# Performance work log

Measured on AMD Instinct MI355X. Metric: run time of the kernel, lower is better.

The kernel has to match this reference:

```python
import jax, jax.numpy as jnp
import numpy as np
import math

EMBED_DIM = 512
DEPTH = 0
HEAD_DIM = EMBED_DIM // 2
LAMBDA_INIT = 0.8 - 0.6 * math.exp(-0.3 * DEPTH)
RMS_EPS = 1e-5


def setup_inputs() -> dict:
    key = jax.random.key(0)
    ks = jax.random.split(key, 10)
    B, NG, NS, E = 8, 4096, 1024, EMBED_DIM
    s = 1.0 / math.sqrt(E)
    return {
        "gene": jax.random.normal(ks[0], (B, NG, E), jnp.float32),
        "substructure": jax.random.normal(ks[1], (B, NS, E), jnp.float32),
        "Wq": jax.random.normal(ks[2], (E, E), jnp.float32) * s,
        "Wk": jax.random.normal(ks[3], (E, E), jnp.float32) * s,
        "Wv": jax.random.normal(ks[4], (E, E), jnp.float32) * s,
        "Wo": jax.random.normal(ks[5], (E, E), jnp.float32) * s,
        "lambda_q1": jax.random.normal(ks[6], (HEAD_DIM,), jnp.float32) * 0.1,
        "lambda_k1": jax.random.normal(ks[7], (HEAD_DIM,), jnp.float32) * 0.1,
        "lambda_q2": jax.random.normal(ks[8], (HEAD_DIM,), jnp.float32) * 0.1,
        "lambda_k2": jax.random.normal(ks[9], (HEAD_DIM,), jnp.float32) * 0.1,
        "rms_weight": jnp.ones((E,), jnp.float32),
    }


def reference(gene, substructure, Wq, Wk, Wv, Wo,
              lambda_q1, lambda_k1, lambda_q2, lambda_k2, rms_weight):
    B, NG, E = gene.shape
    NS = substructure.shape[1]
    h = HEAD_DIM
    scaling = h ** -0.5

    # projections (torch Linear: y = x @ W.T)
    q = (gene @ Wq.T).reshape(B, NG, 2, h).transpose(0, 2, 1, 3)          # [B,2,NG,h]
    k = (substructure @ Wk.T).reshape(B, NS, 2, h).transpose(0, 2, 1, 3)  # [B,2,NS,h]
    v = substructure @ Wv.T                                               # [B,NS,E]

    attn = jax.nn.softmax(jnp.einsum('bhqd,bhkd->bhqk', q * scaling, k), axis=-1)

    lam1 = jnp.exp(jnp.sum(lambda_q1 * lambda_k1))
    lam2 = jnp.exp(jnp.sum(lambda_q2 * lambda_k2))
    lam_full = lam1 - lam2 + LAMBDA_INIT

    diff_attn = attn[:, 0] - lam_full * attn[:, 1]                        # [B,NG,NS]
    out = jnp.einsum('bqk,bke->bqe', diff_attn, v)                        # [B,NG,E]

    # RMSNorm over last dim with affine weight
    out = out * jax.lax.rsqrt(jnp.mean(out * out, axis=-1, keepdims=True) + RMS_EPS) * rms_weight
    out = out * (1.0 - LAMBDA_INIT)
    out = out @ Wo.T
    return out, diff_attn
```

## Files before the change

kernel.cpp:

```cpp
#include <hip/hip_runtime.h>
#include <cstdint>
#include <cstddef>

#define DEVFN __device__ __forceinline__

typedef unsigned short u16;
typedef uint32_t u32;
typedef __attribute__((ext_vector_type(8))) short bf16x8;
typedef __attribute__((ext_vector_type(4))) float f32x4;

constexpr int NB  = 8;
constexpr int NGQ = 4096;
constexpr int NSS = 1024;
constexpr int EE  = 512;
constexpr float SCALING      = 0.0625f;
constexpr float LAMBDA_INIT_C = 0.2f;
constexpr float RMS_EPS_C     = 1e-5f;

DEVFN u16 f2bf(float x) {
  u32 u = __builtin_bit_cast(u32, x);
  u += 0x7FFFu + ((u >> 16) & 1u);
  return (u16)(u >> 16);
}
DEVFN float bf2f(u16 u) { return __builtin_bit_cast(float, (u32)u << 16); }
DEVFN u32 pkf16(float a, float b) {
  _Float16 ha = (_Float16)a, hb = (_Float16)b;
  return (u32)__builtin_bit_cast(u16, ha) | ((u32)__builtin_bit_cast(u16, hb) << 16);
}
DEVFN float f16lo(u32 v) { return (float)__builtin_bit_cast(_Float16, (u16)(v & 0xffffu)); }
DEVFN float f16hi(u32 v) { return (float)__builtin_bit_cast(_Float16, (u16)(v >> 16)); }

typedef const char __attribute__((address_space(1)))* gas_t;
typedef       char __attribute__((address_space(3)))* las_t;
DEVFN void async16(const void* g, void* l) {
  __builtin_amdgcn_global_load_lds((gas_t)g, (las_t)l, 16, 0, 0);
}

__global__ void cvt_kernel(const float* __restrict__ s, u16* __restrict__ d, int n4) {
  int i = blockIdx.x * blockDim.x + threadIdx.x;
  int stride = gridDim.x * blockDim.x;
  for (; i < n4; i += stride) {
    float4 v = ((const float4*)s)[i];
    uint2 p;
    p.x = (u32)f2bf(v.x) | ((u32)f2bf(v.y) << 16);
    p.y = (u32)f2bf(v.z) | ((u32)f2bf(v.w) << 16);
    ((uint2*)d)[i] = p;
  }
}

__global__ void cvt4_kernel(const float* s0, const float* s1, const float* s2, const float* s3,
                            u16* d0, u16* d1, u16* d2, u16* d3, int n4) {
  const float* sp[4] = {s0, s1, s2, s3};
  u16* dp[4] = {d0, d1, d2, d3};
  const float* s = sp[blockIdx.y];
  u16* d = dp[blockIdx.y];
  int i = blockIdx.x * blockDim.x + threadIdx.x;
  int stride = gridDim.x * blockDim.x;
  for (; i < n4; i += stride) {
    float4 v = ((const float4*)s)[i];
    uint2 p;
    p.x = (u32)f2bf(v.x) | ((u32)f2bf(v.y) << 16);
    p.y = (u32)f2bf(v.z) | ((u32)f2bf(v.w) << 16);
    ((uint2*)d)[i] = p;
  }
}

__global__ void lam_kernel(const float* __restrict__ lq1, const float* __restrict__ lk1,
                           const float* __restrict__ lq2, const float* __restrict__ lk2,
                           float* __restrict__ out) {
  int l = threadIdx.x;
  float s1 = 0.f, s2 = 0.f;
  for (int i = l; i < 256; i += 64) {
    s1 += lq1[i] * lk1[i];
    s2 += lq2[i] * lk2[i];
  }
#pragma unroll
  for (int off = 1; off < 64; off <<= 1) {
    s1 += __shfl_xor(s1, off);
    s2 += __shfl_xor(s2, off);
  }
  if (l == 0) out[0] = __expf(s1) - __expf(s2) + LAMBDA_INIT_C;
}

template<int OM>
__global__ __launch_bounds__(256, 2) void gemm_bt(const u16* __restrict__ A,
                                                  const u16* __restrict__ W,
                                                  void* __restrict__ Cv, float oscale) {
  __shared__ u16 As[128 * 64];
  __shared__ u16 Bs[128 * 64];
  const int tid = threadIdx.x;
  const int lane = tid & 63, wid = tid >> 6;
  const int lr = lane & 15, lg = lane >> 4;
  const int m0 = blockIdx.x * 128, n0 = blockIdx.y * 128;
  const int wm = wid >> 1, wn = wid & 1;

  f32x4 acc[4][4];
#pragma unroll
  for (int i = 0; i < 4; ++i)
#pragma unroll
    for (int j = 0; j < 4; ++j) acc[i][j] = (f32x4){0.f, 0.f, 0.f, 0.f};

  const int srow = lane >> 3;
  const int sg   = (lane & 7) ^ srow;

  for (int kt = 0; kt < 512; kt += 64) {
#pragma unroll
    for (int j = 0; j < 4; ++j) {
      int r0 = j * 32 + wid * 8;
      async16(A + (size_t)(m0 + r0 + srow) * 512 + kt + sg * 8, As + r0 * 64);
      async16(W + (size_t)(n0 + r0 + srow) * 512 + kt + sg * 8, Bs + r0 * 64);
    }
    __syncthreads();
#pragma unroll
    for (int kk = 0; kk < 2; ++kk) {
      bf16x8 av[4], bv[4];
#pragma unroll
      for (int f = 0; f < 4; ++f) {
        int rowa = wm * 64 + f * 16 + lr;
        av[f] = *(const bf16x8*)(As + rowa * 64 + (((kk * 4 + lg) ^ (rowa & 7)) * 8));
        int rowb = wn * 64 + f * 16 + lr;
        bv[f] = *(const bf16x8*)(Bs + rowb * 64 + (((kk * 4 + lg) ^ (rowb & 7)) * 8));
      }
#pragma unroll
      for (int mf = 0; mf < 4; ++mf)
#pragma unroll
        for (int nf = 0; nf < 4; ++nf)
          acc[mf][nf] = __builtin_amdgcn_mfma_f32_16x16x32_bf16(av[mf], bv[nf], acc[mf][nf], 0, 0, 0);
    }
    __syncthreads();
  }

  if (OM == 0) {
    u16* C = (u16*)Cv;
#pragma unroll
    for (int mf = 0; mf < 4; ++mf) {
      int row = m0 + wm * 64 + mf * 16 + lg * 4;
#pragma unroll
      for (int nf = 0; nf < 4; ++nf) {
        int col = n0 + wn * 64 + nf * 16 + lr;
#pragma unroll
        for (int r = 0; r < 4; ++r)
          C[(size_t)(row + r) * 512 + col] = f2bf(acc[mf][nf][r] * oscale);
      }
    }
  } else if (OM == 1) {
    u16* C = (u16*)Cv;
#pragma unroll
    for (int mf = 0; mf < 4; ++mf) {
      int m = m0 + wm * 64 + mf * 16 + lg * 4;
      int bb = m >> 10, s = m & 1023;
      int c = s >> 5, s32 = s & 31;
#pragma unroll
      for (int nf = 0; nf < 4; ++nf) {
        int col = n0 + wn * 64 + nf * 16 + lr;
        uint2 v;
        v.x = (u32)f2bf(acc[mf][nf][0]) | ((u32)f2bf(acc[mf][nf][1]) << 16);
        v.y = (u32)f2bf(acc[mf][nf][2]) | ((u32)f2bf(acc[mf][nf][3]) << 16);
        *(uint2*)(C + (size_t)bb * 524288 + (size_t)c * 16384 + col * 32 + s32) = v;
      }
    }
  } else {
    float* C = (float*)Cv;
#pragma unroll
    for (int mf = 0; mf < 4; ++mf) {
      int row = m0 + wm * 64 + mf * 16 + lg * 4;
#pragma unroll
      for (int nf = 0; nf < 4; ++nf) {
        int col = n0 + wn * 64 + nf * 16 + lr;
#pragma unroll
        for (int r = 0; r < 4; ++r)
          C[(size_t)(row + r) * 512 + col] = acc[mf][nf][r];
      }
    }
  }
}

constexpr int CH = 32;
constexpr int NCH = NSS / CH;
constexpr int DSP = 40;

__global__ __launch_bounds__(512, 4) void attn_kernel(
    const u16* __restrict__ Qw, const u16* __restrict__ Kw,
    const u16* __restrict__ Vc, const float* __restrict__ rmsw,
    const float* __restrict__ lamp,
    float* __restrict__ diffp, u16* __restrict__ normed) {
  __shared__ u16 KVu[2][CH * 512];
  __shared__ u16 Ds[64 * DSP];
  __shared__ float redm[2][4][2][16];
  __shared__ float redl[2][4][2][16];
  __shared__ float red2[64][2];

  const int tid = threadIdx.x;
  const int lane = tid & 63, wid = tid >> 6;
  const int qs = wid >> 1, wh = wid & 1;
  const int lr = lane & 15, lg = lane >> 4;
  const int b = blockIdx.x, qt = blockIdx.y;
  const size_t qrb = (size_t)b * NGQ + (size_t)qt * 64;
  const int q = qs * 16 + lr;

  bf16x8 qf[2][8];
  {
    const u16* qp = Qw + (qrb + q) * 512;
#pragma unroll
    for (int hd = 0; hd < 2; ++hd)
#pragma unroll
      for (int kk = 0; kk < 8; ++kk)
        qf[hd][kk] = *(const bf16x8*)(qp + hd * 256 + kk * 32 + lg * 8);
  }
  const float lam = lamp[0];
  u32* stash = (u32*)diffp;
  const size_t sbase = (qrb + q) * (size_t)NSS + wh * 16 + lg * 4;

  const u16* kbase = Kw + (size_t)b * NSS * 512;
  const u16* vbase = Vc + (size_t)b * 524288;
  const int rowk = wh * 16 + lr;
  const int rx = rowk & 7;
  const int vse = lane >> 2;
  const int vsg = (lane & 3) ^ ((lane >> 3) & 3);
  const int vrf = (lr >> 1) & 3;

#pragma unroll
  for (int i = 0; i < 4; ++i) {
    int row = i * 8 + wid;
    async16(kbase + (size_t)row * 512 + (lane ^ (row & 7)) * 8, &KVu[0][row * 512]);
  }
  asm volatile("s_waitcnt vmcnt(0)" ::: "memory");
  __builtin_amdgcn_s_barrier();
  __builtin_amdgcn_sched_barrier(0);

  float mrun[2] = {-3e38f, -3e38f};
  float lrun[2] = {0.f, 0.f};

  for (int c = 0; c < NCH; ++c) {
    if (c + 1 < NCH) {
      const u16* kb = kbase + (size_t)(c + 1) * CH * 512;
#pragma unroll
      for (int i = 0; i < 4; ++i) {
        int row = i * 8 + wid;
        async16(kb + (size_t)row * 512 + (lane ^ (row & 7)) * 8, &KVu[(c + 1) & 1][row * 512]);
      }
    }
    const u16* kp = &KVu[c & 1][rowk * 512];
    f32x4 s0v = {0.f, 0.f, 0.f, 0.f}, s1v = {0.f, 0.f, 0.f, 0.f};
    __builtin_amdgcn_s_setprio(1);
#pragma unroll
    for (int kk = 0; kk < 8; ++kk) {
      bf16x8 kf0 = *(const bf16x8*)(kp + (((kk * 4 + lg) ^ rx) * 8));
      s0v = __builtin_amdgcn_mfma_f32_16x16x32_bf16(kf0, qf[0][kk], s0v, 0, 0, 0);
      bf16x8 kf1 = *(const bf16x8*)(kp + (((32 + kk * 4 + lg) ^ rx) * 8));
      s1v = __builtin_amdgcn_mfma_f32_16x16x32_bf16(kf1, qf[1][kk], s1v, 0, 0, 0);
    }
    __builtin_amdgcn_s_setprio(0);
    {
      float mx = fmaxf(fmaxf(s0v[0], s0v[1]), fmaxf(s0v[2], s0v[3]));
      float mn = fmaxf(mrun[0], mx);
      float sc = __expf(mrun[0] - mn);
      lrun[0] = lrun[0] * sc + __expf(s0v[0] - mn) + __expf(s0v[1] - mn)
                             + __expf(s0v[2] - mn) + __expf(s0v[3] - mn);
      mrun[0] = mn;
      mx = fmaxf(fmaxf(s1v[0], s1v[1]), fmaxf(s1v[2], s1v[3]));
      mn = fmaxf(mrun[1], mx);
      sc = __expf(mrun[1] - mn);
      lrun[1] = lrun[1] * sc + __expf(s1v[0] - mn) + __expf(s1v[1] - mn)
                             + __expf(s1v[2] - mn) + __expf(s1v[3] - mn);
      mrun[1] = mn;
    }
    uint4 pk;
    pk.x = pkf16(s0v[0], s1v[0]);
    pk.y = pkf16(s0v[1], s1v[1]);
    pk.z = pkf16(s0v[2], s1v[2]);
    pk.w = pkf16(s0v[3], s1v[3]);
    *(uint4*)(stash + sbase + (size_t)c * CH) = pk;
    if (c + 1 < NCH) {
      asm volatile("s_waitcnt vmcnt(1)" ::: "memory");
      __builtin_amdgcn_s_barrier();
      __builtin_amdgcn_sched_barrier(0);
    }
  }
  asm volatile("s_waitcnt vmcnt(0)" ::: "memory");
  __syncthreads();

  float Mf[2], Li[2];
#pragma unroll
  for (int hd = 0; hd < 2; ++hd) {
    float m = mrun[hd], l = lrun[hd];
#pragma unroll
    for (int off = 16; off < 64; off <<= 1) {
      float mo = __shfl_xor(m, off);
      float lo = __shfl_xor(l, off);
      float mn = fmaxf(m, mo);
      l = l * __expf(m - mn) + lo * __expf(mo - mn);
      m = mn;
    }
    if (lane < 16) { redm[hd][qs][wh][lane] = m; redl[hd][qs][wh][lane] = l; }
  }
  __syncthreads();
#pragma unroll
  for (int hd = 0; hd < 2; ++hd) {
    float ma = redm[hd][qs][0][lr], la = redl[hd][qs][0][lr];
    float mb = redm[hd][qs][1][lr], lb = redl[hd][qs][1][lr];
    float mn = fmaxf(ma, mb);
    float l = la * __expf(ma - mn) + lb * __expf(mb - mn);
    Mf[hd] = mn;
    Li[hd] = 1.f / l;
  }

  f32x4 oacc[16];
#pragma unroll
  for (int n = 0; n < 16; ++n) oacc[n] = (f32x4){0.f, 0.f, 0.f, 0.f};

#pragma unroll
  for (int i = 0; i < 4; ++i) {
    int k = wid * 4 + i;
    int e = k * 16 + vse;
    async16(vbase + (size_t)e * 32 + vsg * 8, &KVu[0][k * 512]);
  }
  uint4 sp_cur = *(const uint4*)(stash + sbase);
  asm volatile("s_waitcnt vmcnt(0)" ::: "memory");
  __builtin_amdgcn_s_barrier();
  __builtin_amdgcn_sched_barrier(0);

  for (int c = 0; c < NCH; ++c) {
    uint4 sp_nxt = sp_cur;
    if (c + 1 < NCH) {
      const u16* vb = vbase + (size_t)(c + 1) * 16384;
#pragma unroll
      for (int i = 0; i < 4; ++i) {
        int k = wid * 4 + i;
        int e = k * 16 + vse;
        async16(vb + (size_t)e * 32 + vsg * 8, &KVu[(c + 1) & 1][k * 512]);
      }
      sp_nxt = *(const uint4*)(stash + sbase + (size_t)(c + 1) * CH);
    }
    float dd[4];
    dd[0] = __expf(f16lo(sp_cur.x) - Mf[0]) * Li[0] - lam * (__expf(f16hi(sp_cur.x) - Mf[1]) * Li[1]);
    dd[1] = __expf(f16lo(sp_cur.y) - Mf[0]) * Li[0] - lam * (__expf(f16hi(sp_cur.y) - Mf[1]) * Li[1]);
    dd[2] = __expf(f16lo(sp_cur.z) - Mf[0]) * Li[0] - lam * (__expf(f16hi(sp_cur.z) - Mf[1]) * Li[1]);
    dd[3] = __expf(f16lo(sp_cur.w) - Mf[0]) * Li[0] - lam * (__expf(f16hi(sp_cur.w) - Mf[1]) * Li[1]);
    {
      int g16 = wh * 2 + (lg >> 1);
      int offs = q * DSP + ((g16 ^ (q & 3)) * 8) + (lg & 1) * 4;
      uint2 pk2;
      pk2.x = (u32)f2bf(dd[0]) | ((u32)f2bf(dd[1]) << 16);
      pk2.y = (u32)f2bf(dd[2]) | ((u32)f2bf(dd[3]) << 16);
      *(uint2*)(Ds + offs) = pk2;
    }
    asm volatile("s_waitcnt lgkmcnt(0)" ::: "memory");
    __builtin_amdgcn_s_barrier();
    __builtin_amdgcn_sched_barrier(0);
    {
      bf16x8 af = *(const bf16x8*)(Ds + q * DSP + ((lg ^ (q & 3)) * 8));
      const u16* vsb = &KVu[c & 1][0];
      __builtin_amdgcn_s_setprio(1);
#pragma unroll
      for (int n = 0; n < 16; ++n) {
        int e = wh * 256 + n * 16 + lr;
        bf16x8 vf = *(const bf16x8*)(vsb + e * 32 + ((lg ^ vrf) * 8));
        oacc[n] = __builtin_amdgcn_mfma_f32_16x16x32_bf16(af, vf, oacc[n], 0, 0, 0);
      }
      __builtin_amdgcn_s_setprio(0);
    }
    {
      int cq = tid >> 3, s8 = tid & 7;
      int slot = (s8 >> 1) ^ (cq & 3);
      uint2 v = *(const uint2*)(Ds + cq * DSP + slot * 8 + (s8 & 1) * 4);
      float4 f4;
      f4.x = bf2f((u16)(v.x & 0xffffu));
      f4.y = bf2f((u16)(v.x >> 16));
      f4.z = bf2f((u16)(v.y & 0xffffu));
      f4.w = bf2f((u16)(v.y >> 16));
      *(float4*)(diffp + (qrb + cq) * (size_t)NSS + c * CH + s8 * 4) = f4;
    }
    if (c + 1 < NCH) {
      asm volatile("s_waitcnt vmcnt(2)" ::: "memory");
      __builtin_amdgcn_s_barrier();
      __builtin_amdgcn_sched_barrier(0);
    }
    sp_cur = sp_nxt;
  }
  __syncthreads();

  float ssq[4] = {0.f, 0.f, 0.f, 0.f};
#pragma unroll
  for (int n = 0; n < 16; ++n)
#pragma unroll
    for (int r = 0; r < 4; ++r) ssq[r] += oacc[n][r] * oacc[n][r];
#pragma unroll
  for (int off = 1; off < 16; off <<= 1)
#pragma unroll
    for (int r = 0; r < 4; ++r) ssq[r] += __shfl_xor(ssq[r], off);
  if (lr == 0) {
#pragma unroll
    for (int r = 0; r < 4; ++r) red2[qs * 16 + lg * 4 + r][wh] = ssq[r];
  }
  __syncthreads();
  float wv[16];
#pragma unroll
  for (int n = 0; n < 16; ++n) wv[n] = rmsw[wh * 256 + n * 16 + lr] * 0.8f;
#pragma unroll
  for (int r = 0; r < 4; ++r) {
    int row = qs * 16 + lg * 4 + r;
    float tot = red2[row][0] + red2[row][1];
    float rs = rsqrtf(tot * (1.f / 512.f) + RMS_EPS_C);
    u16* np = normed + (qrb + row) * 512 + wh * 256 + lr;
#pragma unroll
    for (int n = 0; n < 16; ++n)
      np[n * 16] = f2bf(oacc[n][r] * rs * wv[n]);
  }
}

extern "C" void kernel_launch(void* const* d_in, const int* in_sizes, int n_in,
                              void* d_out, int out_size, void* d_ws, size_t ws_size,
                              hipStream_t stream) {
  (void)in_sizes; (void)n_in; (void)out_size; (void)ws_size;
  const float* gene = (const float*)d_in[0];
  const float* sub  = (const float*)d_in[1];
  const float* Wq   = (const float*)d_in[2];
  const float* Wk   = (const float*)d_in[3];
  const float* Wv   = (const float*)d_in[4];
  const float* Wo   = (const float*)d_in[5];
  const float* lq1  = (const float*)d_in[6];
  const float* lk1  = (const float*)d_in[7];
  const float* lq2  = (const float*)d_in[8];
  const float* lk2  = (const float*)d_in[9];
  const float* rmsw = (const float*)d_in[10];

  float* outp  = (float*)d_out;
  float* diffp = outp + (size_t)NB * NGQ * EE;

  u16* gene_bf = (u16*)diffp;
  u16* sub_bf  = gene_bf + (size_t)NB * NGQ * EE;
  u16* Wq_bf   = sub_bf  + (size_t)NB * NSS * EE;
  u16* Wk_bf   = Wq_bf + 262144;
  u16* Wv_bf   = Wk_bf + 262144;

  char*  ws   = (char*)d_ws;
  float* lamv = (float*)ws;
  u16* Qw = (u16*)(ws + 64);
  u16* Kw = Qw + (size_t)NB * NGQ * EE;
  u16* Vc = Kw + (size_t)NB * NSS * EE;
  u16* Wo_bf = Vc + (size_t)NB * NSS * EE;
  u16* normed = Qw;

  const int T = 256;
  auto blk = [](int n4) { int b = (n4 + 255) / 256; return b > 2048 ? 2048 : b; };
  cvt_kernel<<<dim3(blk(NB*NGQ*EE/4)), dim3(T), 0, stream>>>(gene, gene_bf, NB*NGQ*EE/4);
  cvt_kernel<<<dim3(blk(NB*NSS*EE/4)), dim3(T), 0, stream>>>(sub,  sub_bf,  NB*NSS*EE/4);
  cvt4_kernel<<<dim3(64, 4), dim3(T), 0, stream>>>(Wq, Wk, Wv, Wo,
                                                   Wq_bf, Wk_bf, Wv_bf, Wo_bf, 65536);
  lam_kernel<<<dim3(1), dim3(64), 0, stream>>>(lq1, lk1, lq2, lk2, lamv);

  gemm_bt<0><<<dim3(256, 4), dim3(256), 0, stream>>>(gene_bf, Wq_bf, Qw, SCALING);
  gemm_bt<0><<<dim3(64, 4),  dim3(256), 0, stream>>>(sub_bf,  Wk_bf, Kw, 1.0f);
  gemm_bt<1><<<dim3(64, 4),  dim3(256), 0, stream>>>(sub_bf,  Wv_bf, Vc, 1.0f);
  attn_kernel<<<dim3(8, 64), dim3(512), 0, stream>>>(Qw, Kw, Vc, rmsw, lamv, diffp, normed);
  gemm_bt<2><<<dim3(256, 4), dim3(256), 0, stream>>>(normed, Wo_bf, outp, 1.0f);
}
```

Baseline: 250.3 us.

## Use exp2 softmax with folded log-normalizer and double-buffer Ds to drop a barrier

Scales Q by log2(e) in the projection GEMM so the softmax can use the hardware exp2 directly. The normalizer is folded into the max as m + log2(l), which removes the per-element multiply by 1/l. The Ds staging tile is double-buffered, so the trailing barrier in the second pass is removed and its vmcnt wait moves to the existing mid-loop barrier. This cuts one workgroup barrier per chunk plus some ALU work, at the cost of extra LDS and a tighter dependency on the exact vmcnt accounting.

```diff
diff --git a/kernel.cpp b/kernel.cpp
--- a/kernel.cpp
+++ b/kernel.cpp
@@ -14,6 +14,7 @@
 constexpr int NSS = 1024;
 constexpr int EE  = 512;
 constexpr float SCALING      = 0.0625f;
+constexpr float LOG2E        = 1.4426950408889634f;
 constexpr float LAMBDA_INIT_C = 0.2f;
 constexpr float RMS_EPS_C     = 1e-5f;
 
@@ -29,6 +30,8 @@
 }
 DEVFN float f16lo(u32 v) { return (float)__builtin_bit_cast(_Float16, (u16)(v & 0xffffu)); }
 DEVFN float f16hi(u32 v) { return (float)__builtin_bit_cast(_Float16, (u16)(v >> 16)); }
+DEVFN float ex2(float x) { return __builtin_amdgcn_exp2f(x); }
+DEVFN float lg2(float x) { return __builtin_amdgcn_logf(x); }
 
 typedef const char __attribute__((address_space(1)))* gas_t;
 typedef       char __attribute__((address_space(3)))* las_t;
@@ -185,7 +188,7 @@
     const float* __restrict__ lamp,
     float* __restrict__ diffp, u16* __restrict__ normed) {
   __shared__ u16 KVu[2][CH * 512];
-  __shared__ u16 Ds[64 * DSP];
+  __shared__ u16 Ds[2][64 * DSP];
   __shared__ float redm[2][4][2][16];
   __shared__ float redl[2][4][2][16];
   __shared__ float red2[64][2];
@@ -254,15 +257,15 @@
     {
       float mx = fmaxf(fmaxf(s0v[0], s0v[1]), fmaxf(s0v[2], s0v[3]));
       float mn = fmaxf(mrun[0], mx);
-      float sc = __expf(mrun[0] - mn);
-      lrun[0] = lrun[0] * sc + __expf(s0v[0] - mn) + __expf(s0v[1] - mn)
-                             + __expf(s0v[2] - mn) + __expf(s0v[3] - mn);
+      float sc = ex2(mrun[0] - mn);
+      lrun[0] = lrun[0] * sc + ex2(s0v[0] - mn) + ex2(s0v[1] - mn)
+                             + ex2(s0v[2] - mn) + ex2(s0v[3] - mn);
       mrun[0] = mn;
       mx = fmaxf(fmaxf(s1v[0], s1v[1]), fmaxf(s1v[2], s1v[3]));
       mn = fmaxf(mrun[1], mx);
-      sc = __expf(mrun[1] - mn);
-      lrun[1] = lrun[1] * sc + __expf(s1v[0] - mn) + __expf(s1v[1] - mn)
-                             + __expf(s1v[2] - mn) + __expf(s1v[3] - mn);
+      sc = ex2(mrun[1] - mn);
+      lrun[1] = lrun[1] * sc + ex2(s1v[0] - mn) + ex2(s1v[1] - mn)
+                             + ex2(s1v[2] - mn) + ex2(s1v[3] - mn);
       mrun[1] = mn;
     }
     uint4 pk;
@@ -280,7 +283,7 @@
   asm volatile("s_waitcnt vmcnt(0)" ::: "memory");
   __syncthreads();
 
-  float Mf[2], Li[2];
+  float Mfp[2];
 #pragma unroll
   for (int hd = 0; hd < 2; ++hd) {
     float m = mrun[hd], l = lrun[hd];
@@ -289,7 +292,7 @@
       float mo = __shfl_xor(m, off);
       float lo = __shfl_xor(l, off);
       float mn = fmaxf(m, mo);
-      l = l * __expf(m - mn) + lo * __expf(mo - mn);
+      l = l * ex2(m - mn) + lo * ex2(mo - mn);
       m = mn;
     }
     if (lane < 16) { redm[hd][qs][wh][lane] = m; redl[hd][qs][wh][lane] = l; }
@@ -300,9 +303,8 @@
     float ma = redm[hd][qs][0][lr], la = redl[hd][qs][0][lr];
     float mb = redm[hd][qs][1][lr], lb = redl[hd][qs][1][lr];
     float mn = fmaxf(ma, mb);
-    float l = la * __expf(ma - mn) + lb * __expf(mb - mn);
-    Mf[hd] = mn;
-    Li[hd] = 1.f / l;
+    float l = la * ex2(ma - mn) + lb * ex2(mb - mn);
+    Mfp[hd] = mn + lg2(l);
   }
 
   f32x4 oacc[16];
@@ -315,12 +317,14 @@
     int e = k * 16 + vse;
     async16(vbase + (size_t)e * 32 + vsg * 8, &KVu[0][k * 512]);
   }
+  __builtin_amdgcn_sched_barrier(0);
   uint4 sp_cur = *(const uint4*)(stash + sbase);
   asm volatile("s_waitcnt vmcnt(0)" ::: "memory");
   __builtin_amdgcn_s_barrier();
   __builtin_amdgcn_sched_barrier(0);
 
   for (int c = 0; c < NCH; ++c) {
+    const int bi = c & 1;
     uint4 sp_nxt = sp_cur;
     if (c + 1 < NCH) {
       const u16* vb = vbase + (size_t)(c + 1) * 16384;
@@ -330,27 +334,28 @@
         int e = k * 16 + vse;
         async16(vb + (size_t)e * 32 + vsg * 8, &KVu[(c + 1) & 1][k * 512]);
       }
+      __builtin_amdgcn_sched_barrier(0);
       sp_nxt = *(const uint4*)(stash + sbase + (size_t)(c + 1) * CH);
     }
     float dd[4];
-    dd[0] = __expf(f16lo(sp_cur.x) - Mf[0]) * Li[0] - lam * (__expf(f16hi(sp_cur.x) - Mf[1]) * Li[1]);
-    dd[1] = __expf(f16lo(sp_cur.y) - Mf[0]) * Li[0] - lam * (__expf(f16hi(sp_cur.y) - Mf[1]) * Li[1]);
-    dd[2] = __expf(f16lo(sp_cur.z) - Mf[0]) * Li[0] - lam * (__expf(f16hi(sp_cur.z) - Mf[1]) * Li[1]);
-    dd[3] = __expf(f16lo(sp_cur.w) - Mf[0]) * Li[0] - lam * (__expf(f16hi(sp_cur.w) - Mf[1]) * Li[1]);
+    dd[0] = ex2(f16lo(sp_cur.x) - Mfp[0]) - lam * ex2(f16hi(sp_cur.x) - Mfp[1]);
+    dd[1] = ex2(f16lo(sp_cur.y) - Mfp[0]) - lam * ex2(f16hi(sp_cur.y) - Mfp[1]);
+    dd[2] = ex2(f16lo(sp_cur.z) - Mfp[0]) - lam * ex2(f16hi(sp_cur.z) - Mfp[1]);
+    dd[3] = ex2(f16lo(sp_cur.w) - Mfp[0]) - lam * ex2(f16hi(sp_cur.w) - Mfp[1]);
     {
       int g16 = wh * 2 + (lg >> 1);
       int offs = q * DSP + ((g16 ^ (q & 3)) * 8) + (lg & 1) * 4;
       uint2 pk2;
       pk2.x = (u32)f2bf(dd[0]) | ((u32)f2bf(dd[1]) << 16);
       pk2.y = (u32)f2bf(dd[2]) | ((u32)f2bf(dd[3]) << 16);
-      *(uint2*)(Ds + offs) = pk2;
-    }
-    asm volatile("s_waitcnt lgkmcnt(0)" ::: "memory");
+      *(uint2*)(&Ds[bi][0] + offs) = pk2;
+    }
+    asm volatile("s_waitcnt vmcnt(6) lgkmcnt(0)" ::: "memory");
     __builtin_amdgcn_s_barrier();
     __builtin_amdgcn_sched_barrier(0);
     {
-      bf16x8 af = *(const bf16x8*)(Ds + q * DSP + ((lg ^ (q & 3)) * 8));
-      const u16* vsb = &KVu[c & 1][0];
+      bf16x8 af = *(const bf16x8*)(&Ds[bi][0] + q * DSP + ((lg ^ (q & 3)) * 8));
+      const u16* vsb = &KVu[bi][0];
       __builtin_amdgcn_s_setprio(1);
 #pragma unroll
       for (int n = 0; n < 16; ++n) {
@@ -363,18 +368,13 @@
     {
       int cq = tid >> 3, s8 = tid & 7;
       int slot = (s8 >> 1) ^ (cq & 3);
-      uint2 v = *(const uint2*)(Ds + cq * DSP + slot * 8 + (s8 & 1) * 4);
+      uint2 v = *(const uint2*)(&Ds[bi][0] + cq * DSP + slot * 8 + (s8 & 1) * 4);
       float4 f4;
       f4.x = bf2f((u16)(v.x & 0xffffu));
       f4.y = bf2f((u16)(v.x >> 16));
       f4.z = bf2f((u16)(v.y & 0xffffu));
       f4.w = bf2f((u16)(v.y >> 16));
       *(float4*)(diffp + (qrb + cq) * (size_t)NSS + c * CH + s8 * 4) = f4;
-    }
-    if (c + 1 < NCH) {
-      asm volatile("s_waitcnt vmcnt(2)" ::: "memory");
-      __builtin_amdgcn_s_barrier();
-      __builtin_amdgcn_sched_barrier(0);
     }
     sp_cur = sp_nxt;
   }
@@ -450,7 +450,7 @@
                                                    Wq_bf, Wk_bf, Wv_bf, Wo_bf, 65536);
   lam_kernel<<<dim3(1), dim3(64), 0, stream>>>(lq1, lk1, lq2, lk2, lamv);
 
-  gemm_bt<0><<<dim3(256, 4), dim3(256), 0, stream>>>(gene_bf, Wq_bf, Qw, SCALING);
+  gemm_bt<0><<<dim3(256, 4), dim3(256), 0, stream>>>(gene_bf, Wq_bf, Qw, SCALING * LOG2E);
   gemm_bt<0><<<dim3(64, 4),  dim3(256), 0, stream>>>(sub_bf,  Wk_bf, Kw, 1.0f);
   gemm_bt<1><<<dim3(64, 4),  dim3(256), 0, stream>>>(sub_bf,  Wv_bf, Vc, 1.0f);
   attn_kernel<<<dim3(8, 64), dim3(512), 0, stream>>>(Qw, Kw, Vc, rmsw, lamv, diffp, normed);
```

New measurement: 244.2 us. 2.5% less time.
